# Performance work log

Hardware: AMD Instinct MI355X
Metric: run time of the kernel (lower is better)

## Reference

```python
import jax, jax.numpy as jnp
import numpy as np

H = W = 64      # patch grid (shape)
WS = 8          # window_size
SHIFT = 4       # shift_size (SW-MSA)
HEAD_DIM = 32
N = WS * WS     # tokens per window


def _rel_position_index(ws):
    coords = np.stack(np.meshgrid(np.arange(ws), np.arange(ws), indexing='ij'))  # (2, ws, ws)
    cf = coords.reshape(2, -1)
    rel = cf[:, :, None] - cf[:, None, :]            # (2, N, N)
    rel = rel.transpose(1, 2, 0).astype(np.int64)    # (N, N, 2)
    rel[..., 0] += ws - 1
    rel[..., 1] += ws - 1
    rel[..., 0] *= 2 * ws - 1
    return (rel[..., 0] + rel[..., 1]).astype(np.int32)  # (N, N), values in [0,(2ws-1)^2)


def _shift_mask(h, w, ws, shift):
    # Swin cyclic-shift attention mask: (num_windows, N, N) with 0 / -100
    img = np.zeros((h, w), dtype=np.float32)
    cnt = 0
    slices = (slice(0, -ws), slice(-ws, -shift), slice(-shift, None))
    for hs in slices:
        for ws_ in slices:
            img[hs, ws_] = cnt
            cnt += 1
    win = img.reshape(h // ws, ws, w // ws, ws).transpose(0, 2, 1, 3).reshape(-1, ws * ws)
    diff = win[:, None, :] - win[:, :, None]
    return np.where(diff != 0, np.float32(-100.0), np.float32(0.0))


def setup_inputs() -> dict:
    key = jax.random.key(0)
    ks = jax.random.split(key, 6)
    dim = 384
    B = 32
    sd = 1.0 / np.sqrt(dim)
    return {
        'x': jax.random.normal(ks[0], (B, H * W, dim), jnp.float32),
        'qkv_w': jax.random.normal(ks[1], (dim, 3 * dim), jnp.float32) * sd,
        'qkv_b': jnp.zeros((3 * dim,), jnp.float32),
        'proj_w': jax.random.normal(ks[2], (dim, dim), jnp.float32) * sd,
        'proj_b': jnp.zeros((dim,), jnp.float32),
        'bias_table': jax.random.normal(ks[3], ((2 * WS - 1) ** 2, dim // HEAD_DIM), jnp.float32) * 0.02,
        'rel_index': jnp.asarray(_rel_position_index(WS)),
    }


def reference(x, qkv_w, qkv_b, proj_w, proj_b, bias_table, rel_index):
    B, L, C = x.shape
    heads = C // HEAD_DIM
    scale = HEAD_DIM ** -0.5
    nh, nw = H // WS, W // WS

    xg = x.reshape(B, H, W, C)
    if SHIFT > 0:
        xg = jnp.roll(xg, shift=(-SHIFT, -SHIFT), axis=(1, 2))

    # window partition -> (B*nWin, N, C)
    xw = xg.reshape(B, nh, WS, nw, WS, C).transpose(0, 1, 3, 2, 4, 5).reshape(B * nh * nw, N, C)

    qkv = xw @ qkv_w + qkv_b                              # (Bw, N, 3C)
    q, k, v = jnp.split(qkv, 3, axis=-1)
    def heads_first(t):
        return t.reshape(-1, N, heads, HEAD_DIM).transpose(0, 2, 1, 3)  # (Bw, h, N, d)
    q, k, v = heads_first(q), heads_first(k), heads_first(v)

    attn = jnp.einsum('bhnd,bhmd->bhnm', q * scale, k)    # (Bw, h, N, N)
    bias = bias_table[rel_index]                          # (N, N, h)
    attn = attn + bias.transpose(2, 0, 1)[None]

    if SHIFT > 0:
        mask = jnp.asarray(_shift_mask(H, W, WS, SHIFT))  # (nWin, N, N), trace-time constant
        attn = attn.reshape(B, nh * nw, heads, N, N) + mask[None, :, None]
        attn = attn.reshape(B * nh * nw, heads, N, N)

    attn = jax.nn.softmax(attn, axis=-1)
    out = jnp.einsum('bhnm,bhmd->bhnd', attn, v)          # (Bw, h, N, d)
    out = out.transpose(0, 2, 1, 3).reshape(B * nh * nw, N, C)
    out = out @ proj_w + proj_b

    # window reverse
    out = out.reshape(B, nh, nw, WS, WS, C).transpose(0, 1, 3, 2, 4, 5).reshape(B, H, W, C)
    if SHIFT > 0:
        out = jnp.roll(out, shift=(SHIFT, SHIFT), axis=(1, 2))
    return out.reshape(B, L, C)
```

## Files before the change

### kernel.cpp

```cpp
#include <hip/hip_runtime.h>
#include <hip/hip_bf16.h>

#define CDIM 384
#define NQKV 1152
#define HEADS 12
#define SHIFT_ 4
#define SCALE_Q 0.17677669529663687f

typedef __attribute__((ext_vector_type(8))) short bf16x8;
typedef __attribute__((ext_vector_type(4))) float f32x4;
typedef __attribute__((ext_vector_type(4))) float float4_t;
typedef __attribute__((ext_vector_type(4))) unsigned u32x4;
typedef __attribute__((ext_vector_type(2))) unsigned u32x2;

__device__ inline short f2bf(float f) {
    union { float f; unsigned u; } v; v.f = f;
    unsigned r = v.u + 0x7FFFu + ((v.u >> 16) & 1u);
    return (short)(r >> 16);
}

__device__ inline unsigned cvtpk(float lo, float hi) {
    unsigned r;
    asm("v_cvt_pk_bf16_f32 %0, %1, %2" : "=v"(r) : "v"(lo), "v"(hi));
    return r;
}

__device__ inline bf16x8 mk8(unsigned w0, unsigned w1, unsigned w2, unsigned w3) {
    u32x4 t = {w0, w1, w2, w3};
    return __builtin_bit_cast(bf16x8, t);
}

__device__ inline bf16x8 pack8(float4_t a, float4_t b) {
    return mk8(cvtpk(a[0], a[1]), cvtpk(a[2], a[3]),
               cvtpk(b[0], b[1]), cvtpk(b[2], b[3]));
}

__device__ inline bf16x8 regroup(unsigned p0, unsigned p1, unsigned p2,
                                 unsigned p3, int lane) {
    int lhi = (lane >> 4) & 3;
    int s0 = (lane & 15) + ((lhi & 1) ? 32 : 0);
    int s1 = s0 + 16;
    unsigned a0 = __shfl(p0, s0), b0 = __shfl(p2, s0);
    unsigned a1 = __shfl(p1, s0), b1 = __shfl(p3, s0);
    unsigned a2 = __shfl(p0, s1), b2 = __shfl(p2, s1);
    unsigned a3 = __shfl(p1, s1), b3 = __shfl(p3, s1);
    bool hi = lhi >= 2;
    return mk8(hi ? b0 : a0, hi ? b1 : a1, hi ? b2 : a2, hi ? b3 : a3);
}

__device__ inline void gl16(const short* g, const short* l) {
    __builtin_amdgcn_global_load_lds((const __attribute__((address_space(1))) void*)g,
                                     (__attribute__((address_space(3))) void*)l, 16, 0, 0);
}

__device__ inline int invswz(int c) {
    int b2 = (c >> 2) & 1, b3 = (c >> 3) & 1, b4 = (c >> 4) & 1;
    return (c & ~7) | ((b2 ^ b4) << 2) | (((((c >> 1) & 1)) ^ b3) << 1) | ((c & 1) ^ b2 ^ b4);
}

__device__ inline int region_id(int wIdx, int tok) {
    int gh = ((wIdx >> 3) << 3) + (tok >> 3);
    int gw = (wIdx & 7) * 8 + (tok & 7);
    int rh = gh < 56 ? 0 : (gh < 60 ? 1 : 2);
    int rw = gw < 56 ? 0 : (gw < 60 ? 1 : 2);
    return rh * 3 + rw;
}

__device__ inline int crow(int row) { return row * 136 + (row >> 3) * 8; }

__device__ inline size_t xrow(int mg) {
    int tok = mg & 63, win = mg >> 6;
    int b = win >> 6, wIdx = win & 63;
    int gh = ((wIdx >> 3) << 3) + (tok >> 3);
    int gw = (wIdx & 7) * 8 + (tok & 7);
    int sh_ = (gh + SHIFT_) & 63, sw_ = (gw + SHIFT_) & 63;
    return (size_t)(b * 4096 + sh_ * 64 + sw_) * CDIM;
}

__global__ void prep_kernel(const float* __restrict__ qkv_w,
                            const float* __restrict__ proj_w,
                            const float* __restrict__ bias_table,
                            const int* __restrict__ rel_index,
                            short* __restrict__ qkvwt,
                            short* __restrict__ projwt,
                            float* __restrict__ biasP) {
    int t = blockIdx.x * 256 + threadIdx.x;
    if (t < NQKV * CDIM) {
        int n = t / CDIM, k = t - n * CDIM;
        qkvwt[t] = f2bf(qkv_w[k * NQKV + n]);
    }
    if (t < CDIM * CDIM) {
        int n = t / CDIM, k = t - n * CDIM;
        projwt[t] = f2bf(proj_w[k * CDIM + n]);
    }
    if (t < HEADS * 16 * 64 * 4) {
        int r = t & 3, lane = (t >> 2) & 63, g = (t >> 8) & 15, h = t >> 12;
        int kt = g >> 2, qt = g & 3;
        int key = kt * 16 + (lane >> 4) * 4 + r;
        int query = qt * 16 + (lane & 15);
        biasP[t] = bias_table[rel_index[query * 64 + key] * HEADS + h];
    }
}

__global__ __launch_bounds__(256) void gemm_qkv(
    const float* __restrict__ x, const short* __restrict__ wt,
    const float* __restrict__ qkv_b, short* __restrict__ qkbuf,
    short* __restrict__ vT)
{
    __shared__ alignas(16) char smemb[35072];
    short* As = (short*)smemb;
    short* Bs = As + 4096;
    short* Cst = (short*)smemb;
    int tid = threadIdx.x;
    int hw = blockIdx.x;
    int lb = (hw & 7) * 1152 + (hw >> 3);
    int bm = lb / 9, bn = lb - bm * 9;
    int m0 = bm * 128, n0 = bn * 128;

    int lane = tid & 63, wv = tid >> 6;
    int c0 = wv * 128 + lane, c1 = c0 + 64;
    const float* Asrc0 = x + xrow(m0 + (c0 >> 2)) + (c0 & 3) * 8;
    const float* Asrc1 = x + xrow(m0 + (c1 >> 2)) + (c1 & 3) * 8;
    short* Aw0 = As + (c0 ^ ((c0 >> 2) & 7)) * 8;
    short* Aw1 = As + (c1 ^ ((c1 >> 2) & 7)) * 8;
    int l0 = invswz(c0), l1 = invswz(c1);
    const short* Bg0 = wt + (size_t)(n0 + (l0 >> 2)) * CDIM + (l0 & 3) * 8;
    const short* Bg1 = wt + (size_t)(n0 + (l1 >> 2)) * CDIM + (l1 & 3) * 8;
    const short* Bdst0 = (const short*)((const char*)Bs + wv * 2048);
    const short* Bdst1 = (const short*)((const char*)Bs + wv * 2048 + 1024);

    int wr = wv >> 1, wc = wv & 1;
    int lrow = lane & 15, lhi = lane >> 4;
    int arow = wr * 64 + lrow, brow = wc * 64 + lrow;
    const short* ard = As + ((((arow * 64 + lhi * 16)) ^ ((lrow & 7) << 4)) >> 1);
    const short* brd = Bs + ((((brow * 64 + lhi * 16)) ^ ((lrow & 7) << 4)) >> 1);

    f32x4 zero = {0.f, 0.f, 0.f, 0.f};
    f32x4 acc[4][4];
    #pragma unroll
    for (int i = 0; i < 4; i++)
        #pragma unroll
        for (int j = 0; j < 4; j++) acc[i][j] = zero;

    #pragma unroll
    for (int ks = 0; ks < 12; ks++) {
        int k0 = ks * 32;
        float4_t a00 = *(const float4_t*)(Asrc0 + k0);
        float4_t a01 = *(const float4_t*)(Asrc0 + k0 + 4);
        float4_t a10 = *(const float4_t*)(Asrc1 + k0);
        float4_t a11 = *(const float4_t*)(Asrc1 + k0 + 4);
        gl16(Bg0 + k0, Bdst0);
        gl16(Bg1 + k0, Bdst1);
        *(bf16x8*)Aw0 = pack8(a00, a01);
        *(bf16x8*)Aw1 = pack8(a10, a11);
        __syncthreads();
        bf16x8 af[4], bfr[4];
        #pragma unroll
        for (int t = 0; t < 4; t++) af[t]  = *(const bf16x8*)(ard + t * 512);
        #pragma unroll
        for (int t = 0; t < 4; t++) bfr[t] = *(const bf16x8*)(brd + t * 512);
        #pragma unroll
        for (int i = 0; i < 4; i++)
            #pragma unroll
            for (int j = 0; j < 4; j++)
                acc[i][j] = __builtin_amdgcn_mfma_f32_16x16x32_bf16(af[i], bfr[j], acc[i][j], 0, 0, 0);
        __syncthreads();
    }
    #pragma unroll
    for (int tj = 0; tj < 4; tj++) {
        int col = wc * 64 + tj * 16 + lrow;
        int cg = n0 + col;
        float bias = qkv_b[cg];
        float sc = (cg < CDIM) ? SCALE_Q : 1.0f;
        #pragma unroll
        for (int ti = 0; ti < 4; ti++) {
            int row0 = wr * 64 + ti * 16 + lhi * 4;
            #pragma unroll
            for (int r = 0; r < 4; r++)
                Cst[crow(row0 + r) + col] = f2bf((acc[ti][tj][r] + bias) * sc);
        }
    }
    __syncthreads();
    if (bn < 6) {
        #pragma unroll
        for (int i = 0; i < 8; i++) {
            int rr = i * 16 + (tid >> 4);
            int cc = (tid & 15) * 8;
            bf16x8 v = *(const bf16x8*)(Cst + crow(rr) + cc);
            __builtin_nontemporal_store(v,
                (bf16x8*)(qkbuf + (size_t)(m0 + rr) * 768 + n0 + cc));
        }
    } else {
        #pragma unroll
        for (int it = 0; it < 8; it++) {
            int t = it * 256 + tid;
            int col = t >> 4, tk8 = t & 15;
            bf16x8 v;
            #pragma unroll
            for (int j = 0; j < 8; j++)
                v[j] = Cst[crow(tk8 * 8 + j) + col];
            int win = bm * 2 + (tk8 >> 3);
            int head = (bn - 6) * 4 + (col >> 5);
            int dim = col & 31;
            __builtin_nontemporal_store(v,
                (bf16x8*)(vT + (((size_t)win * HEADS + head) * 32 + dim) * 64 + (tk8 & 7) * 8));
        }
    }
}

__global__ __launch_bounds__(256) void attn_reg(
    const short* __restrict__ qkbuf, const short* __restrict__ vT,
    const float* __restrict__ biasP, short* __restrict__ attno)
{
    int tid = threadIdx.x;
    int lane = tid & 63, wv = tid >> 6;
    int lrow = lane & 15, lhi = lane >> 4;
    int w = blockIdx.x;
    int wIdx = w & 63;
    bool needmask = ((wIdx >> 3) == 7) || ((wIdx & 7) == 7);

    int rq[4], rk[4][4];
    #pragma unroll
    for (int qt = 0; qt < 4; qt++) rq[qt] = region_id(wIdx, qt * 16 + lrow);
    #pragma unroll
    for (int kt = 0; kt < 4; kt++)
        #pragma unroll
        for (int r = 0; r < 4; r++)
            rk[kt][r] = region_id(wIdx, kt * 16 + lhi * 4 + r);

    f32x4 zero = {0.f, 0.f, 0.f, 0.f};
    const short* qbase = qkbuf + (size_t)(w * 64) * 768;

    for (int hi = 0; hi < 3; hi++) {
        int h = wv * 3 + hi;
        bf16x8 kf[4];
        #pragma unroll
        for (int kt = 0; kt < 4; kt++)
            kf[kt] = __builtin_nontemporal_load(
                (const bf16x8*)(qbase + (size_t)(kt * 16 + lrow) * 768 + CDIM + h * 32 + lhi * 8));
        bf16x8 pa[4][2];
        #pragma unroll
        for (int qt = 0; qt < 4; qt++) {
            bf16x8 qf = __builtin_nontemporal_load(
                (const bf16x8*)(qbase + (size_t)(qt * 16 + lrow) * 768 + h * 32 + lhi * 8));
            f32x4 st[4];
            __builtin_amdgcn_s_setprio(1);
            #pragma unroll
            for (int kt = 0; kt < 4; kt++)
                st[kt] = __builtin_amdgcn_mfma_f32_16x16x32_bf16(kf[kt], qf, zero, 0, 0, 0);
            __builtin_amdgcn_s_setprio(0);
            float pv[16]; float sum = 0.f;
            #pragma unroll
            for (int kt = 0; kt < 4; kt++) {
                f32x4 bb = *(const f32x4*)(biasP + (((size_t)h * 16 + kt * 4 + qt) * 64 + lane) * 4);
                #pragma unroll
                for (int r = 0; r < 4; r++) {
                    float p = __expf(st[kt][r] + bb[r]);
                    p = (needmask && (rq[qt] != rk[kt][r])) ? 0.f : p;
                    pv[kt * 4 + r] = p; sum += p;
                }
            }
            sum += __shfl_xor(sum, 16);
            sum += __shfl_xor(sum, 32);
            float rcp = 1.0f / sum;
            unsigned a0 = cvtpk(pv[0] * rcp, pv[1] * rcp);
            unsigned a1 = cvtpk(pv[2] * rcp, pv[3] * rcp);
            unsigned a2 = cvtpk(pv[4] * rcp, pv[5] * rcp);
            unsigned a3 = cvtpk(pv[6] * rcp, pv[7] * rcp);
            pa[qt][0] = regroup(a0, a1, a2, a3, lane);
            a0 = cvtpk(pv[8] * rcp,  pv[9] * rcp);
            a1 = cvtpk(pv[10] * rcp, pv[11] * rcp);
            a2 = cvtpk(pv[12] * rcp, pv[13] * rcp);
            a3 = cvtpk(pv[14] * rcp, pv[15] * rcp);
            pa[qt][1] = regroup(a0, a1, a2, a3, lane);
        }
        const short* vb = vT + ((size_t)w * HEADS + h) * 32 * 64;
        bf16x8 vfrag[2][2];
        #pragma unroll
        for (int ks2 = 0; ks2 < 2; ks2++)
            #pragma unroll
            for (int dt = 0; dt < 2; dt++)
                vfrag[ks2][dt] = __builtin_nontemporal_load(
                    (const bf16x8*)(vb + (size_t)(dt * 16 + lrow) * 64 + ks2 * 32 + lhi * 8));
        f32x4 ao2[4][2];
        #pragma unroll
        for (int qt = 0; qt < 4; qt++) { ao2[qt][0] = zero; ao2[qt][1] = zero; }
        __builtin_amdgcn_s_setprio(1);
        #pragma unroll
        for (int ks2 = 0; ks2 < 2; ks2++)
            #pragma unroll
            for (int qt = 0; qt < 4; qt++) {
                ao2[qt][0] = __builtin_amdgcn_mfma_f32_16x16x32_bf16(vfrag[ks2][0], pa[qt][ks2], ao2[qt][0], 0, 0, 0);
                ao2[qt][1] = __builtin_amdgcn_mfma_f32_16x16x32_bf16(vfrag[ks2][1], pa[qt][ks2], ao2[qt][1], 0, 0, 0);
            }
        __builtin_amdgcn_s_setprio(0);
        short* abase = attno + (size_t)(w * 64) * CDIM + h * 32 + lhi * 4;
        #pragma unroll
        for (int qt = 0; qt < 4; qt++) {
            int token = qt * 16 + lrow;
            short* p0 = abase + (size_t)token * CDIM;
            u32x2 s0, s1;
            s0[0] = cvtpk(ao2[qt][0][0], ao2[qt][0][1]);
            s0[1] = cvtpk(ao2[qt][0][2], ao2[qt][0][3]);
            s1[0] = cvtpk(ao2[qt][1][0], ao2[qt][1][1]);
            s1[1] = cvtpk(ao2[qt][1][2], ao2[qt][1][3]);
            __builtin_nontemporal_store(s0, (u32x2*)(p0));
            __builtin_nontemporal_store(s1, (u32x2*)(p0 + 16));
        }
    }
}

__global__ __launch_bounds__(256) void gemm_proj(
    const short* __restrict__ a, const short* __restrict__ wt,
    const float* __restrict__ proj_b, float* __restrict__ out)
{
    __shared__ alignas(16) short As[4096];
    __shared__ alignas(16) short Bs[4096];
    int tid = threadIdx.x;
    int hw = blockIdx.x;
    int lb = (hw & 7) * 384 + (hw >> 3);
    int bm = lb / 3, bn = lb - bm * 3;
    int m0 = bm * 128, n0 = bn * 128;

    int lane = tid & 63, wv = tid >> 6;
    int c0 = wv * 128 + lane, c1 = c0 + 64;
    int l0 = invswz(c0), l1 = invswz(c1);
    const short* Ag0 = a + (size_t)(m0 + (l0 >> 2)) * CDIM + (l0 & 3) * 8;
    const short* Ag1 = a + (size_t)(m0 + (l1 >> 2)) * CDIM + (l1 & 3) * 8;
    const short* Bg0 = wt + (size_t)(n0 + (l0 >> 2)) * CDIM + (l0 & 3) * 8;
    const short* Bg1 = wt + (size_t)(n0 + (l1 >> 2)) * CDIM + (l1 & 3) * 8;
    const short* Adst0 = (const short*)((const char*)As + wv * 2048);
    const short* Adst1 = (const short*)((const char*)As + wv * 2048 + 1024);
    const short* Bdst0 = (const short*)((const char*)Bs + wv * 2048);
    const short* Bdst1 = (const short*)((const char*)Bs + wv * 2048 + 1024);

    int wr = wv >> 1, wc = wv & 1;
    int lrow = lane & 15, lhi = lane >> 4;
    int arow = wr * 64 + lrow, brow = wc * 64 + lrow;
    const short* ard = As + ((((arow * 64 + lhi * 16)) ^ ((lrow & 7) << 4)) >> 1);
    const short* brd = Bs + ((((brow * 64 + lhi * 16)) ^ ((lrow & 7) << 4)) >> 1);

    f32x4 zero = {0.f, 0.f, 0.f, 0.f};
    f32x4 acc[4][4];
    #pragma unroll
    for (int i = 0; i < 4; i++)
        #pragma unroll
        for (int j = 0; j < 4; j++) acc[i][j] = zero;

    for (int k0 = 0; k0 < CDIM; k0 += 32) {
        gl16(Ag0 + k0, Adst0);
        gl16(Bg0 + k0, Bdst0);
        gl16(Ag1 + k0, Adst1);
        gl16(Bg1 + k0, Bdst1);
        __syncthreads();
        bf16x8 af[4], bfr[4];
        #pragma unroll
        for (int t = 0; t < 4; t++) af[t]  = *(const bf16x8*)(ard + t * 512);
        #pragma unroll
        for (int t = 0; t < 4; t++) bfr[t] = *(const bf16x8*)(brd + t * 512);
        #pragma unroll
        for (int i = 0; i < 4; i++)
            #pragma unroll
            for (int j = 0; j < 4; j++)
                acc[i][j] = __builtin_amdgcn_mfma_f32_16x16x32_bf16(af[i], bfr[j], acc[i][j], 0, 0, 0);
        __syncthreads();
    }
    #pragma unroll
    for (int ti = 0; ti < 4; ti++) {
        #pragma unroll
        for (int r = 0; r < 4; r++) {
            int m = m0 + wr * 64 + ti * 16 + lhi * 4 + r;
            int b = m >> 12, wIdx = (m >> 6) & 63, tok = m & 63;
            int gh = ((wIdx >> 3) << 3) + (tok >> 3);
            int gw = (wIdx & 7) * 8 + (tok & 7);
            int ih = (gh + SHIFT_) & 63, iw = (gw + SHIFT_) & 63;
            size_t ob = ((size_t)(b << 12) + ih * 64 + iw) * CDIM;
            #pragma unroll
            for (int tj = 0; tj < 4; tj++) {
                int col = n0 + wc * 64 + tj * 16 + lrow;
                float v = acc[ti][tj][r] + proj_b[col];
                __builtin_nontemporal_store(v, &out[ob + col]);
            }
        }
    }
}

extern "C" void kernel_launch(void* const* d_in, const int* in_sizes, int n_in,
                              void* d_out, int out_size, void* d_ws, size_t ws_size,
                              hipStream_t stream) {
    const float* x          = (const float*)d_in[0];
    const float* qkv_w      = (const float*)d_in[1];
    const float* qkv_b      = (const float*)d_in[2];
    const float* proj_w     = (const float*)d_in[3];
    const float* proj_b     = (const float*)d_in[4];
    const float* bias_table = (const float*)d_in[5];
    const int*   rel_index  = (const int*)d_in[6];
    float* out = (float*)d_out;
    char* ws = (char*)d_ws;

    short* qkvwt = (short*)(ws);
    short* projwt = (short*)(ws + 884736);
    float* biasP  = (float*)(ws + 1179648);
    short* qkbuf  = (short*)(ws + 1376256);
    short* vT     = (short*)(ws + 202702848);
    short* attno  = (short*)(ws + 303366144);

    prep_kernel<<<1728, 256, 0, stream>>>(qkv_w, proj_w, bias_table, rel_index,
                                          qkvwt, projwt, biasP);
    gemm_qkv<<<9216, 256, 0, stream>>>(x, qkvwt, qkv_b, qkbuf, vT);
    attn_reg<<<2048, 256, 0, stream>>>(qkbuf, vT, biasP, attno);
    gemm_proj<<<3072, 256, 0, stream>>>(attno, projwt, proj_b, out);
}
```

Baseline: 471.6 us.

## Double-buffer LDS tiles in QKV and projection GEMMs with one barrier per step

```diff
diff --git a/kernel.cpp b/kernel.cpp
--- a/kernel.cpp
+++ b/kernel.cpp
@@ -109,7 +109,7 @@
 {
     __shared__ alignas(16) char smemb[35072];
     short* As = (short*)smemb;
-    short* Bs = As + 4096;
+    short* Bs = As + 8192;
     short* Cst = (short*)smemb;
     int tid = threadIdx.x;
     int hw = blockIdx.x;
@@ -126,8 +126,8 @@
     int l0 = invswz(c0), l1 = invswz(c1);
     const short* Bg0 = wt + (size_t)(n0 + (l0 >> 2)) * CDIM + (l0 & 3) * 8;
     const short* Bg1 = wt + (size_t)(n0 + (l1 >> 2)) * CDIM + (l1 & 3) * 8;
-    const short* Bdst0 = (const short*)((const char*)Bs + wv * 2048);
-    const short* Bdst1 = (const short*)((const char*)Bs + wv * 2048 + 1024);
+    short* Bdst0 = Bs + wv * 1024;
+    short* Bdst1 = Bdst0 + 512;
 
     int wr = wv >> 1, wc = wv & 1;
     int lrow = lane & 15, lhi = lane >> 4;
@@ -142,28 +142,47 @@
         #pragma unroll
         for (int j = 0; j < 4; j++) acc[i][j] = zero;
 
+    {
+        float4_t p0 = *(const float4_t*)(Asrc0);
+        float4_t p1 = *(const float4_t*)(Asrc0 + 4);
+        float4_t p2 = *(const float4_t*)(Asrc1);
+        float4_t p3 = *(const float4_t*)(Asrc1 + 4);
+        gl16(Bg0, Bdst0);
+        gl16(Bg1, Bdst1);
+        *(bf16x8*)Aw0 = pack8(p0, p1);
+        *(bf16x8*)Aw1 = pack8(p2, p3);
+    }
+    __syncthreads();
+
     #pragma unroll
     for (int ks = 0; ks < 12; ks++) {
-        int k0 = ks * 32;
-        float4_t a00 = *(const float4_t*)(Asrc0 + k0);
-        float4_t a01 = *(const float4_t*)(Asrc0 + k0 + 4);
-        float4_t a10 = *(const float4_t*)(Asrc1 + k0);
-        float4_t a11 = *(const float4_t*)(Asrc1 + k0 + 4);
-        gl16(Bg0 + k0, Bdst0);
-        gl16(Bg1 + k0, Bdst1);
-        *(bf16x8*)Aw0 = pack8(a00, a01);
-        *(bf16x8*)Aw1 = pack8(a10, a11);
-        __syncthreads();
+        int cur = (ks & 1) * 4096, nxt = 4096 - cur;
+        float4_t p0, p1, p2, p3;
+        if (ks < 11) {
+            int k1 = (ks + 1) * 32;
+            gl16(Bg0 + k1, Bdst0 + nxt);
+            gl16(Bg1 + k1, Bdst1 + nxt);
+            p0 = *(const float4_t*)(Asrc0 + k1);
+            p1 = *(const float4_t*)(Asrc0 + k1 + 4);
+            p2 = *(const float4_t*)(Asrc1 + k1);
+            p3 = *(const float4_t*)(Asrc1 + k1 + 4);
+        }
         bf16x8 af[4], bfr[4];
         #pragma unroll
-        for (int t = 0; t < 4; t++) af[t]  = *(const bf16x8*)(ard + t * 512);
-        #pragma unroll
-        for (int t = 0; t < 4; t++) bfr[t] = *(const bf16x8*)(brd + t * 512);
+        for (int t = 0; t < 4; t++) af[t]  = *(const bf16x8*)(ard + cur + t * 512);
+        #pragma unroll
+        for (int t = 0; t < 4; t++) bfr[t] = *(const bf16x8*)(brd + cur + t * 512);
+        __builtin_amdgcn_s_setprio(1);
         #pragma unroll
         for (int i = 0; i < 4; i++)
             #pragma unroll
             for (int j = 0; j < 4; j++)
                 acc[i][j] = __builtin_amdgcn_mfma_f32_16x16x32_bf16(af[i], bfr[j], acc[i][j], 0, 0, 0);
+        __builtin_amdgcn_s_setprio(0);
+        if (ks < 11) {
+            *(bf16x8*)(Aw0 + nxt) = pack8(p0, p1);
+            *(bf16x8*)(Aw1 + nxt) = pack8(p2, p3);
+        }
         __syncthreads();
     }
     #pragma unroll
@@ -314,8 +333,8 @@
     const short* __restrict__ a, const short* __restrict__ wt,
     const float* __restrict__ proj_b, float* __restrict__ out)
 {
-    __shared__ alignas(16) short As[4096];
-    __shared__ alignas(16) short Bs[4096];
+    __shared__ alignas(16) short As[8192];
+    __shared__ alignas(16) short Bs[8192];
     int tid = threadIdx.x;
     int hw = blockIdx.x;
     int lb = (hw & 7) * 384 + (hw >> 3);
@@ -329,10 +348,10 @@
     const short* Ag1 = a + (size_t)(m0 + (l1 >> 2)) * CDIM + (l1 & 3) * 8;
     const short* Bg0 = wt + (size_t)(n0 + (l0 >> 2)) * CDIM + (l0 & 3) * 8;
     const short* Bg1 = wt + (size_t)(n0 + (l1 >> 2)) * CDIM + (l1 & 3) * 8;
-    const short* Adst0 = (const short*)((const char*)As + wv * 2048);
-    const short* Adst1 = (const short*)((const char*)As + wv * 2048 + 1024);
-    const short* Bdst0 = (const short*)((const char*)Bs + wv * 2048);
-    const short* Bdst1 = (const short*)((const char*)Bs + wv * 2048 + 1024);
+    short* Adst0 = As + wv * 1024;
+    short* Adst1 = Adst0 + 512;
+    short* Bdst0 = Bs + wv * 1024;
+    short* Bdst1 = Bdst0 + 512;
 
     int wr = wv >> 1, wc = wv & 1;
     int lrow = lane & 15, lhi = lane >> 4;
@@ -347,22 +366,34 @@
         #pragma unroll
         for (int j = 0; j < 4; j++) acc[i][j] = zero;
 
-    for (int k0 = 0; k0 < CDIM; k0 += 32) {
-        gl16(Ag0 + k0, Adst0);
-        gl16(Bg0 + k0, Bdst0);
-        gl16(Ag1 + k0, Adst1);
-        gl16(Bg1 + k0, Bdst1);
-        __syncthreads();
+    gl16(Ag0, Adst0);
+    gl16(Bg0, Bdst0);
+    gl16(Ag1, Adst1);
+    gl16(Bg1, Bdst1);
+    __syncthreads();
+
+    #pragma unroll
+    for (int ks = 0; ks < 12; ks++) {
+        int cur = (ks & 1) * 4096, nxt = 4096 - cur;
+        if (ks < 11) {
+            int k1 = (ks + 1) * 32;
+            gl16(Ag0 + k1, Adst0 + nxt);
+            gl16(Bg0 + k1, Bdst0 + nxt);
+            gl16(Ag1 + k1, Adst1 + nxt);
+            gl16(Bg1 + k1, Bdst1 + nxt);
+        }
         bf16x8 af[4], bfr[4];
         #pragma unroll
-        for (int t = 0; t < 4; t++) af[t]  = *(const bf16x8*)(ard + t * 512);
-        #pragma unroll
-        for (int t = 0; t < 4; t++) bfr[t] = *(const bf16x8*)(brd + t * 512);
+        for (int t = 0; t < 4; t++) af[t]  = *(const bf16x8*)(ard + cur + t * 512);
+        #pragma unroll
+        for (int t = 0; t < 4; t++) bfr[t] = *(const bf16x8*)(brd + cur + t * 512);
+        __builtin_amdgcn_s_setprio(1);
         #pragma unroll
         for (int i = 0; i < 4; i++)
             #pragma unroll
             for (int j = 0; j < 4; j++)
                 acc[i][j] = __builtin_amdgcn_mfma_f32_16x16x32_bf16(af[i], bfr[j], acc[i][j], 0, 0, 0);
+        __builtin_amdgcn_s_setprio(0);
         __syncthreads();
     }
     #pragma unroll
```

Result: faster. 424.4 us (-10.0%).
